# Kernel optimization log

Measured on AMD Instinct MI355X. Metric: run time of the kernel, lower is better.

The kernel has to match this reference:

```python
import jax, jax.numpy as jnp
import numpy as np

N, E, D, ED, H = 4096, 262144, 256, 64, 8
HD = D // H


def _ln(x, g, b, eps=1e-5):
    mu = jnp.mean(x, axis=-1, keepdims=True)
    var = jnp.mean((x - mu) ** 2, axis=-1, keepdims=True)
    return (x - mu) * jax.lax.rsqrt(var + eps) * g + b


def setup_inputs() -> dict:
    key = jax.random.key(0)
    ks = jax.random.split(key, 16)
    p = lambda k, s: (0.02 * jax.random.normal(k, s, dtype=jnp.float32))
    return {
        'x': jax.random.normal(ks[0], (N, D), dtype=jnp.float32),
        'edge_index': jax.random.randint(ks[1], (2, E), 0, N, dtype=jnp.int64),
        'edge_attr': jax.random.normal(ks[2], (E, ED), dtype=jnp.float32),
        'eps': jnp.zeros((), dtype=jnp.float32),  # GINEConv train_eps initial value 0
        'Wl': p(ks[3], (ED, D)), 'bl': jnp.zeros((D,), jnp.float32),
        'W1': p(ks[4], (D, D)), 'b1': jnp.zeros((D,), jnp.float32),
        'W2': p(ks[5], (D, D)), 'b2': jnp.zeros((D,), jnp.float32),
        'ln_l_g': jnp.ones((D,), jnp.float32), 'ln_l_b': jnp.zeros((D,), jnp.float32),
        'in_w': p(ks[6], (3 * D, D)), 'in_b': jnp.zeros((3 * D,), jnp.float32),
        'out_w': p(ks[7], (D, D)), 'out_b': jnp.zeros((D,), jnp.float32),
        'ln_a_g': jnp.ones((D,), jnp.float32), 'ln_a_b': jnp.zeros((D,), jnp.float32),
        'Wf1': p(ks[8], (D, 2 * D)), 'bf1': jnp.zeros((2 * D,), jnp.float32),
        'Wf2': p(ks[9], (2 * D, D)), 'bf2': jnp.zeros((D,), jnp.float32),
        'ln_f_g': jnp.ones((D,), jnp.float32), 'ln_f_b': jnp.zeros((D,), jnp.float32),
    }


def reference(x, edge_index, edge_attr, eps, Wl, bl, W1, b1, W2, b2,
              ln_l_g, ln_l_b, in_w, in_b, out_w, out_b, ln_a_g, ln_a_b,
              Wf1, bf1, Wf2, bf2, ln_f_g, ln_f_b):
    n = x.shape[0]
    src, dst = edge_index[0], edge_index[1]
    # --- GINEConv: msg = relu(x_j + lin(edge_attr)), sum-aggregate, MLP((1+eps)x + agg)
    msg = jax.nn.relu(x[src] + edge_attr @ Wl + bl)            # [E, D]
    agg = jax.ops.segment_sum(msg, dst, num_segments=n)        # [N, D]
    h = (1.0 + eps) * x + agg
    h = jax.nn.elu(h @ W1 + b1) @ W2 + b2                      # local_mlp
    x = x + jax.nn.elu(_ln(h, ln_l_g, ln_l_b))                 # local residual (dropout=eval)
    # --- MultiheadAttention (single batch of all nodes)
    qkv = x @ in_w.T + in_b                                    # [N, 3D]
    q, k, v = jnp.split(qkv, 3, axis=-1)
    q = q.reshape(n, H, HD)
    k = k.reshape(n, H, HD)
    v = v.reshape(n, H, HD)
    scores = jnp.einsum('qhd,khd->hqk', q, k) / jnp.sqrt(jnp.float32(HD))
    attn = jax.nn.softmax(scores, axis=-1)
    o = jnp.einsum('hqk,khd->qhd', attn, v).reshape(n, D)
    o = o @ out_w.T + out_b
    x = x + _ln(o, ln_a_g, ln_a_b)
    # --- FFN (exact GELU as in torch nn.GELU default)
    f = jax.nn.gelu(x @ Wf1 + bf1, approximate=False) @ Wf2 + bf2
    x = x + _ln(f, ln_f_g, ln_f_b)
    return x
```

## Files before the change

kernel.cpp:

```cpp
#include <hip/hip_runtime.h>
#include <cstddef>

#define D 256
#define H 8
#define HD 32
#define ED 64
#define TPB 4

typedef __attribute__((ext_vector_type(8))) short short8;
typedef __attribute__((ext_vector_type(4))) short short4v;
typedef __attribute__((ext_vector_type(4))) float floatx4;

__device__ inline short f2bf(float f) {
    unsigned u = __float_as_uint(f);
    unsigned r = (u + 0x7fffu + ((u >> 16) & 1u)) >> 16;
    return (short)r;
}

template<int ACT> __device__ inline float act_f(float v) {
    if (ACT == 1) return fmaxf(v, 0.f);
    if (ACT == 2) return v > 0.f ? v : expm1f(v);
    if (ACT == 3) return 0.5f * v * (1.f + erff(v * 0.70710678118654752f));
    return v;
}

__device__ inline float wave_sum(float v) {
#pragma unroll
    for (int off = 32; off > 0; off >>= 1) v += __shfl_xor(v, off, 64);
    return v;
}

__global__ void prep_kernel(
        const float* __restrict__ Wl, const float* __restrict__ W1,
        const float* __restrict__ W2, const float* __restrict__ in_w,
        const float* __restrict__ outw, const float* __restrict__ Wf1,
        const float* __restrict__ Wf2, const float* __restrict__ x,
        const float* __restrict__ eps,
        short* __restrict__ WlT, short* __restrict__ W1bt, short* __restrict__ W2bt,
        short* __restrict__ inwbt, short* __restrict__ outwbt,
        short* __restrict__ Wf1bt, short* __restrict__ Wf2bt,
        int* __restrict__ cnt, float* __restrict__ h, int N, int NF) {
    int idx = blockIdx.x * 256 + threadIdx.x;
    if (idx < 16384) { int n = idx >> 6, k = idx & 63; WlT[idx] = f2bf(Wl[k * 256 + n]); return; }
    idx -= 16384;
    if (idx < 65536) { int n = idx >> 8, k = idx & 255; W1bt[idx] = f2bf(W1[k * 256 + n]); return; }
    idx -= 65536;
    if (idx < 65536) { int n = idx >> 8, k = idx & 255; W2bt[idx] = f2bf(W2[k * 256 + n]); return; }
    idx -= 65536;
    if (idx < 196608) { inwbt[idx] = f2bf(in_w[idx]); return; }
    idx -= 196608;
    if (idx < 65536) { outwbt[idx] = f2bf(outw[idx]); return; }
    idx -= 65536;
    if (idx < 131072) { int n = idx >> 8, k = idx & 255; Wf1bt[idx] = f2bf(Wf1[k * 512 + n]); return; }
    idx -= 131072;
    if (idx < 131072) { int n = idx >> 9, k = idx & 511; Wf2bt[idx] = f2bf(Wf2[k * 256 + n]); return; }
    idx -= 131072;
    if (idx < N) { cnt[idx] = 0; return; }
    idx -= N;
    if (idx < NF) { h[idx] = (1.f + eps[0]) * x[idx]; }
}

__global__ void hist_kernel(const int* __restrict__ ei, int* __restrict__ cnt, int E) {
    int e = blockIdx.x * 256 + threadIdx.x;
    if (e < E) atomicAdd(&cnt[ei[E + e]], 1);
}

__global__ __launch_bounds__(1024) void scan_kernel(int* __restrict__ cnt,
                                                    int* __restrict__ offs) {
    __shared__ int s[1024];
    int tid = threadIdx.x;
    int4 c = *(int4*)&cnt[tid * 4];
    int sum = c.x + c.y + c.z + c.w;
    s[tid] = sum;
    __syncthreads();
    for (int off = 1; off < 1024; off <<= 1) {
        int v = (tid >= off) ? s[tid - off] : 0;
        __syncthreads();
        s[tid] += v;
        __syncthreads();
    }
    int ex = s[tid] - sum;
    int o1 = ex + c.x, o2 = o1 + c.y, o3 = o2 + c.z;
    offs[tid * 4] = ex; offs[tid * 4 + 1] = o1;
    offs[tid * 4 + 2] = o2; offs[tid * 4 + 3] = o3;
    cnt[tid * 4] = ex; cnt[tid * 4 + 1] = o1;
    cnt[tid * 4 + 2] = o2; cnt[tid * 4 + 3] = o3;
    if (tid == 1023) offs[4096] = s[1023];
}

__global__ void scatter_kernel(const int* __restrict__ ei, int* __restrict__ cursor,
                               int* __restrict__ perm, int* __restrict__ srcp,
                               int* __restrict__ dstp, int E) {
    int e = blockIdx.x * 256 + threadIdx.x;
    if (e < E) {
        int d = ei[E + e];
        int pos = atomicAdd(&cursor[d], 1);
        perm[pos] = e;
        srcp[pos] = ei[e];
        dstp[pos] = d;
    }
}

__global__ __launch_bounds__(256) void edge_fused_kernel(
        const float* __restrict__ ea, const short* __restrict__ WlT,
        const float* __restrict__ bl, const float* __restrict__ x,
        const int* __restrict__ perm, const int* __restrict__ srcp,
        const int* __restrict__ dstp, float* __restrict__ h) {
    __shared__ __align__(16) short ea_s[2][64 * 72];
    int tid = threadIdx.x;
    int wave = tid >> 6, lane = tid & 63;
    int mm = lane & 15, quad = lane >> 4;
    int base_e = blockIdx.x * (64 * TPB);

    int myperm[TPB], mysrc[TPB], mydst[TPB];
#pragma unroll
    for (int t = 0; t < TPB; t++) {
        myperm[t] = perm[base_e + t * 64 + lane];
        mysrc[t]  = srcp[base_e + t * 64 + lane];
        mydst[t]  = dstp[base_e + t * 64 + lane];
    }
    short8 af[4][2];
#pragma unroll
    for (int t = 0; t < 4; t++)
#pragma unroll
        for (int q2 = 0; q2 < 2; q2++)
            af[t][q2] = *(const short8*)&WlT[(wave * 64 + t * 16 + mm) * 64 + q2 * 32 + quad * 8];
    float4 blv[4];
#pragma unroll
    for (int t = 0; t < 4; t++)
        blv[t] = *(const float4*)&bl[wave * 64 + t * 16 + quad * 4];

    {
        float4 r[4];
#pragma unroll
        for (int p = 0; p < 4; p++) {
            int slot = tid + p * 256;
            int row = slot >> 4, c4 = slot & 15;
            int prow = __shfl(myperm[0], row);
            r[p] = *(const float4*)&ea[(size_t)prow * ED + c4 * 4];
        }
#pragma unroll
        for (int p = 0; p < 4; p++) {
            int slot = tid + p * 256;
            int row = slot >> 4, c4 = slot & 15;
            short4v s; s[0] = f2bf(r[p].x); s[1] = f2bf(r[p].y); s[2] = f2bf(r[p].z); s[3] = f2bf(r[p].w);
            *(short4v*)&ea_s[0][row * 72 + c4 * 4] = s;
        }
    }
    __syncthreads();

#pragma unroll
    for (int t = 0; t < TPB; t++) {
        const int buf = t & 1;
        float4 pre[4];
        if (t + 1 < TPB) {
#pragma unroll
            for (int p = 0; p < 4; p++) {
                int slot = tid + p * 256;
                int row = slot >> 4, c4 = slot & 15;
                int prow = __shfl(myperm[t + 1], row);
                pre[p] = *(const float4*)&ea[(size_t)prow * ED + c4 * 4];
            }
        }
        floatx4 acc[4][4];
#pragma unroll
        for (int et = 0; et < 4; et++)
#pragma unroll
            for (int tt = 0; tt < 4; tt++) acc[et][tt] = (floatx4){0.f, 0.f, 0.f, 0.f};
#pragma unroll
        for (int et = 0; et < 4; et++) {
            short8 bf0 = *(const short8*)&ea_s[buf][(et * 16 + mm) * 72 + quad * 8];
            short8 bf1 = *(const short8*)&ea_s[buf][(et * 16 + mm) * 72 + 32 + quad * 8];
#pragma unroll
            for (int tt = 0; tt < 4; tt++) {
                acc[et][tt] = __builtin_amdgcn_mfma_f32_16x16x32_bf16(af[tt][0], bf0, acc[et][tt], 0, 0, 0);
                acc[et][tt] = __builtin_amdgcn_mfma_f32_16x16x32_bf16(af[tt][1], bf1, acc[et][tt], 0, 0, 0);
            }
        }
#pragma unroll
        for (int et = 0; et < 4; et++) {
            int srci = __shfl(mysrc[t], et * 16 + mm);
            const float* xrow = x + (size_t)srci * D + wave * 64 + quad * 4;
#pragma unroll
            for (int tt = 0; tt < 4; tt++) {
                float4 xv = *(const float4*)(xrow + tt * 16);
                acc[et][tt][0] = fmaxf(acc[et][tt][0] + blv[tt].x + xv.x, 0.f);
                acc[et][tt][1] = fmaxf(acc[et][tt][1] + blv[tt].y + xv.y, 0.f);
                acc[et][tt][2] = fmaxf(acc[et][tt][2] + blv[tt].z + xv.z, 0.f);
                acc[et][tt][3] = fmaxf(acc[et][tt][3] + blv[tt].w + xv.w, 0.f);
            }
        }
        int prevd = __shfl_up(mydst[t], 1);
        bool bnd = (lane == 0) || (mydst[t] != prevd);
        unsigned long long m = __ballot(bnd);
        while (m) {
            int segstart = (int)__builtin_ctzll(m);
            m &= m - 1;
            int segend = m ? (int)__builtin_ctzll(m) : 64;
            int segdst = __shfl(mydst[t], segstart);
            bool in0 = (0 * 16 + mm >= segstart) & (0 * 16 + mm < segend);
            bool in1 = (1 * 16 + mm >= segstart) & (1 * 16 + mm < segend);
            bool in2 = (2 * 16 + mm >= segstart) & (2 * 16 + mm < segend);
            bool in3 = (3 * 16 + mm >= segstart) & (3 * 16 + mm < segend);
            float* hrow = h + (size_t)segdst * D + wave * 64;
#pragma unroll
            for (int tt = 0; tt < 4; tt++) {
#pragma unroll
                for (int j = 0; j < 4; j++) {
                    float v = (in0 ? acc[0][tt][j] : 0.f) + (in1 ? acc[1][tt][j] : 0.f)
                            + (in2 ? acc[2][tt][j] : 0.f) + (in3 ? acc[3][tt][j] : 0.f);
                    v += __shfl_xor(v, 1);
                    v += __shfl_xor(v, 2);
                    v += __shfl_xor(v, 4);
                    v += __shfl_xor(v, 8);
                    if (mm == 0) atomicAdd(&hrow[tt * 16 + quad * 4 + j], v);
                }
            }
        }
        if (t + 1 < TPB) {
#pragma unroll
            for (int p = 0; p < 4; p++) {
                int slot = tid + p * 256;
                int row = slot >> 4, c4 = slot & 15;
                short4v s; s[0] = f2bf(pre[p].x); s[1] = f2bf(pre[p].y);
                s[2] = f2bf(pre[p].z); s[3] = f2bf(pre[p].w);
                *(short4v*)&ea_s[1 - buf][row * 72 + c4 * 4] = s;
            }
            __syncthreads();
        }
    }
}

#define GSTR 40
template<int ACT>
__global__ __launch_bounds__(256) void gemm_bf16_kernel(
        const float* __restrict__ A, const short* __restrict__ Bt,
        const float* __restrict__ bias, float* __restrict__ C,
        int M, int K, int Nc) {
    __shared__ __align__(16) short As[64 * GSTR];
    __shared__ __align__(16) short Bs[64 * GSTR];
    int tid = threadIdx.x;
    int wave = tid >> 6, lane = tid & 63;
    int mm = lane & 15, quad = lane >> 4;
    int wm = wave >> 1, wn = wave & 1;
    int m0 = blockIdx.y * 64, n0 = blockIdx.x * 64;
    floatx4 acc[2][2];
#pragma unroll
    for (int i = 0; i < 2; i++)
#pragma unroll
        for (int j = 0; j < 2; j++) acc[i][j] = (floatx4){0.f, 0.f, 0.f, 0.f};
    for (int k0 = 0; k0 < K; k0 += 32) {
#pragma unroll
        for (int p = 0; p < 2; p++) {
            int slot = tid + p * 256;
            int row = slot >> 3, c4 = slot & 7;
            float4 v = *(const float4*)&A[(size_t)(m0 + row) * K + k0 + c4 * 4];
            short4v s; s[0] = f2bf(v.x); s[1] = f2bf(v.y); s[2] = f2bf(v.z); s[3] = f2bf(v.w);
            *(short4v*)&As[row * GSTR + c4 * 4] = s;
        }
        {
            int row = tid >> 2, seg = tid & 3;
            short8 v = *(const short8*)&Bt[(size_t)(n0 + row) * K + k0 + seg * 8];
            *(short8*)&Bs[row * GSTR + seg * 8] = v;
        }
        __syncthreads();
        short8 af[2], bf[2];
#pragma unroll
        for (int t = 0; t < 2; t++) {
            af[t] = *(const short8*)&As[(wm * 32 + t * 16 + mm) * GSTR + quad * 8];
            bf[t] = *(const short8*)&Bs[(wn * 32 + t * 16 + mm) * GSTR + quad * 8];
        }
#pragma unroll
        for (int i = 0; i < 2; i++)
#pragma unroll
            for (int j = 0; j < 2; j++)
                acc[i][j] = __builtin_amdgcn_mfma_f32_16x16x32_bf16(af[i], bf[j], acc[i][j], 0, 0, 0);
        __syncthreads();
    }
#pragma unroll
    for (int i = 0; i < 2; i++) {
#pragma unroll
        for (int j = 0; j < 2; j++) {
            int ncol = n0 + wn * 32 + j * 16 + mm;
            float bv = bias[ncol];
#pragma unroll
            for (int r = 0; r < 4; r++) {
                int mrow = m0 + wm * 32 + i * 16 + quad * 4 + r;
                C[(size_t)mrow * Nc + ncol] = act_f<ACT>(acc[i][j][r] + bv);
            }
        }
    }
}

template<int ACT>
__global__ __launch_bounds__(256) void ln_res_kernel(
        const float* __restrict__ t, const float* __restrict__ res,
        const float* __restrict__ g, const float* __restrict__ b,
        float* __restrict__ out) {
    __shared__ float red[8];
    int row = blockIdx.x, tid = threadIdx.x;
    float v = t[(size_t)row * D + tid];
    int wid = tid >> 6, lane = tid & 63;
    float s = wave_sum(v);
    if (lane == 0) red[wid] = s;
    __syncthreads();
    float mu = (red[0] + red[1] + red[2] + red[3]) * (1.f / D);
    float dv = v - mu;
    float s2 = wave_sum(dv * dv);
    if (lane == 0) red[4 + wid] = s2;
    __syncthreads();
    float var = (red[4] + red[5] + red[6] + red[7]) * (1.f / D);
    float y = dv * rsqrtf(var + 1e-5f) * g[tid] + b[tid];
    y = act_f<ACT>(y);
    out[(size_t)row * D + tid] = res[(size_t)row * D + tid] + y;
}

#define KSTR 40
#define VSTR 136
#define ATILE 128
__global__ __launch_bounds__(256) void attn_mfma_kernel(
        const float* __restrict__ qkv, float* __restrict__ po,
        float* __restrict__ pm, float* __restrict__ pl, int N, int KC_) {
    __shared__ __align__(16) short Ks[ATILE * KSTR];
    __shared__ __align__(16) short VTs[HD * VSTR];
    const int tid = threadIdx.x;
    const int wave = tid >> 6, lane = tid & 63;
    const int mm = lane & 15, quad = lane >> 4;
    const int h = blockIdx.y, c = blockIdx.z;
    const int qbase = blockIdx.x * 64 + wave * 16;
    const float scale = 0.17677669529663687f;

    short8 qf;
    {
        const float* qrow = qkv + (size_t)(qbase + mm) * (3 * D) + h * HD + quad * 8;
        float4 a = *(const float4*)qrow;
        float4 b = *(const float4*)(qrow + 4);
        qf[0] = f2bf(a.x * scale); qf[1] = f2bf(a.y * scale);
        qf[2] = f2bf(a.z * scale); qf[3] = f2bf(a.w * scale);
        qf[4] = f2bf(b.x * scale); qf[5] = f2bf(b.y * scale);
        qf[6] = f2bf(b.z * scale); qf[7] = f2bf(b.w * scale);
    }
    floatx4 accA = {0.f, 0.f, 0.f, 0.f};
    floatx4 accB = {0.f, 0.f, 0.f, 0.f};
    float m_r = -1e30f, l_r = 0.f;

    const int kchunk = N / KC_;
    const int kstart = c * kchunk;
    const int krow0 = ((mm >> 2) << 3) | (mm & 3);

    for (int t0 = 0; t0 < kchunk; t0 += ATILE) {
#pragma unroll
        for (int p = 0; p < 4; p++) {
            int slot = tid + p * 256;
            int kr = slot >> 3, e4 = slot & 7;
            const float* krow = qkv + (size_t)(kstart + t0 + kr) * (3 * D) + D + h * HD + e4 * 4;
            float4 kv = *(const float4*)krow;
            short4v ks;
            ks[0] = f2bf(kv.x); ks[1] = f2bf(kv.y); ks[2] = f2bf(kv.z); ks[3] = f2bf(kv.w);
            *(short4v*)&Ks[kr * KSTR + e4 * 4] = ks;
            const float* vrow = qkv + (size_t)(kstart + t0 + kr) * (3 * D) + 2 * D + h * HD + e4 * 4;
            float4 vv = *(const float4*)vrow;
            VTs[(e4 * 4 + 0) * VSTR + kr] = f2bf(vv.x);
            VTs[(e4 * 4 + 1) * VSTR + kr] = f2bf(vv.y);
            VTs[(e4 * 4 + 2) * VSTR + kr] = f2bf(vv.z);
            VTs[(e4 * 4 + 3) * VSTR + kr] = f2bf(vv.w);
        }
        __syncthreads();
#pragma unroll
        for (int s = 0; s < ATILE / 32; s++) {
            int sb = s * 32;
            short8 kf0 = *(const short8*)&Ks[(sb + krow0) * KSTR + quad * 8];
            short8 kf1 = *(const short8*)&Ks[(sb + krow0 + 4) * KSTR + quad * 8];
            floatx4 zero = {0.f, 0.f, 0.f, 0.f};
            floatx4 s0 = __builtin_amdgcn_mfma_f32_16x16x32_bf16(kf0, qf, zero, 0, 0, 0);
            floatx4 s1 = __builtin_amdgcn_mfma_f32_16x16x32_bf16(kf1, qf, zero, 0, 0, 0);
            float mx = fmaxf(fmaxf(fmaxf(s0[0], s0[1]), fmaxf(s0[2], s0[3])),
                             fmaxf(fmaxf(s1[0], s1[1]), fmaxf(s1[2], s1[3])));
            mx = fmaxf(mx, __shfl_xor(mx, 16));
            mx = fmaxf(mx, __shfl_xor(mx, 32));
            float nm = fmaxf(m_r, mx);
            float alpha = __expf(m_r - nm);
            float p0[4], p1[4], ls = 0.f;
#pragma unroll
            for (int j = 0; j < 4; j++) {
                p0[j] = __expf(s0[j] - nm);
                p1[j] = __expf(s1[j] - nm);
                ls += p0[j] + p1[j];
            }
            ls += __shfl_xor(ls, 16);
            ls += __shfl_xor(ls, 32);
            l_r = l_r * alpha + ls;
            m_r = nm;
            short8 pf;
#pragma unroll
            for (int j = 0; j < 4; j++) { pf[j] = f2bf(p0[j]); pf[4 + j] = f2bf(p1[j]); }
#pragma unroll
            for (int j = 0; j < 4; j++) { accA[j] *= alpha; accB[j] *= alpha; }
            short8 vf0 = *(const short8*)&VTs[mm * VSTR + sb + quad * 8];
            short8 vf1 = *(const short8*)&VTs[(mm + 16) * VSTR + sb + quad * 8];
            accA = __builtin_amdgcn_mfma_f32_16x16x32_bf16(vf0, pf, accA, 0, 0, 0);
            accB = __builtin_amdgcn_mfma_f32_16x16x32_bf16(vf1, pf, accB, 0, 0, 0);
        }
        __syncthreads();
    }
    size_t NH = (size_t)N * H;
    int qi = qbase + mm;
    size_t nh = (size_t)qi * H + h;
    if (lane < 16) {
        pm[(size_t)c * NH + nh] = m_r;
        pl[(size_t)c * NH + nh] = l_r;
    }
    float* op = po + ((size_t)c * NH + nh) * HD;
#pragma unroll
    for (int j = 0; j < 4; j++) {
        op[quad * 4 + j] = accA[j];
        op[16 + quad * 4 + j] = accB[j];
    }
}

__global__ __launch_bounds__(256) void attn_combine_kernel(
        const float* __restrict__ po, const float* __restrict__ pm,
        const float* __restrict__ pl, float* __restrict__ obuf, int N, int KC_) {
    int idx = blockIdx.x * 256 + threadIdx.x;
    int d = idx & (HD - 1);
    int nh = idx >> 5;
    size_t NH = (size_t)N * H;
    float M = -1e30f;
    for (int cc = 0; cc < KC_; cc++) M = fmaxf(M, pm[(size_t)cc * NH + nh]);
    float l = 0.f, o = 0.f;
    for (int cc = 0; cc < KC_; cc++) {
        float a = __expf(pm[(size_t)cc * NH + nh] - M);
        l += a * pl[(size_t)cc * NH + nh];
        o += a * po[((size_t)cc * NH + nh) * HD + d];
    }
    int n = nh >> 3, h = nh & (H - 1);
    obuf[(size_t)n * D + h * HD + d] = o / l;
}

extern "C" void kernel_launch(void* const* d_in, const int* in_sizes, int n_in,
                              void* d_out, int out_size, void* d_ws, size_t ws_size,
                              hipStream_t stream) {
    const float* x    = (const float*)d_in[0];
    const int*   ei   = (const int*)d_in[1];
    const float* ea   = (const float*)d_in[2];
    const float* eps  = (const float*)d_in[3];
    const float* Wl   = (const float*)d_in[4];
    const float* bl   = (const float*)d_in[5];
    const float* W1   = (const float*)d_in[6];
    const float* b1   = (const float*)d_in[7];
    const float* W2   = (const float*)d_in[8];
    const float* b2   = (const float*)d_in[9];
    const float* lnlg = (const float*)d_in[10];
    const float* lnlb = (const float*)d_in[11];
    const float* in_w = (const float*)d_in[12];
    const float* in_b = (const float*)d_in[13];
    const float* outw = (const float*)d_in[14];
    const float* outb = (const float*)d_in[15];
    const float* lnag = (const float*)d_in[16];
    const float* lnab = (const float*)d_in[17];
    const float* Wf1  = (const float*)d_in[18];
    const float* bf1  = (const float*)d_in[19];
    const float* Wf2  = (const float*)d_in[20];
    const float* bf2  = (const float*)d_in[21];
    const float* lnfg = (const float*)d_in[22];
    const float* lnfb = (const float*)d_in[23];
    float* out = (float*)d_out;

    const int N = in_sizes[0] / D;
    const int E = in_sizes[1] / 2;
    const size_t NF = (size_t)N * D;
    const size_t NH = (size_t)N * H;

    const int KCsel = 4;
    size_t floatEnd = (4 + (size_t)KCsel) * NF + 2 * (size_t)KCsel * NH;
    size_t offB = (floatEnd * 4 + 15) & ~(size_t)15;
    size_t intCount = (size_t)N + 3 * (size_t)E + (size_t)(N + 1);
    size_t wltOff = (offB + intCount * 4 + 15) & ~(size_t)15;

    float* w = (float*)d_ws;
    float* x1   = w;
    float* qkv  = w + NF;
    float* h    = w + 4 * NF;
    float* t1   = w + 5 * NF;
    float* t2   = w + 6 * NF;
    float* po   = w + 4 * NF;
    float* pm   = w + (4 + (size_t)KCsel) * NF;
    float* pl   = pm + (size_t)KCsel * NH;
    float* obuf = w + NF;
    float* t3   = w + 2 * NF;
    float* x2   = w + 3 * NF;
    float* f1   = w + 4 * NF;
    float* f2   = w + 6 * NF;

    char* base = (char*)d_ws;
    int* ibase  = (int*)(base + offB);
    int* cnt    = ibase;
    int* perm   = ibase + N;
    int* srcp   = perm + E;
    int* dstp   = srcp + E;
    int* offs   = dstp + E;
    short* WlT    = (short*)(base + wltOff);
    short* W1bt   = WlT + 16384;
    short* W2bt   = W1bt + 65536;
    short* inwbt  = W2bt + 65536;
    short* outwbt = inwbt + 196608;
    short* Wf1bt  = outwbt + 65536;
    short* Wf2bt  = Wf1bt + 131072;

    {
        int total = 671744 + N + (int)NF;
        prep_kernel<<<(total + 255) / 256, 256, 0, stream>>>(
            Wl, W1, W2, in_w, outw, Wf1, Wf2, x, eps,
            WlT, W1bt, W2bt, inwbt, outwbt, Wf1bt, Wf2bt, cnt, h, N, (int)NF);
    }
    hist_kernel<<<(E + 255) / 256, 256, 0, stream>>>(ei, cnt, E);
    scan_kernel<<<1, 1024, 0, stream>>>(cnt, offs);
    scatter_kernel<<<(E + 255) / 256, 256, 0, stream>>>(ei, cnt, perm, srcp, dstp, E);
    edge_fused_kernel<<<E / (64 * TPB), 256, 0, stream>>>(ea, WlT, bl, x, perm, srcp, dstp, h);
    gemm_bf16_kernel<2><<<dim3(D / 64, N / 64), 256, 0, stream>>>(h, W1bt, b1, t1, N, D, D);
    gemm_bf16_kernel<0><<<dim3(D / 64, N / 64), 256, 0, stream>>>(t1, W2bt, b2, t2, N, D, D);
    ln_res_kernel<2><<<N, 256, 0, stream>>>(t2, x, lnlg, lnlb, x1);
    gemm_bf16_kernel<0><<<dim3(3 * D / 64, N / 64), 256, 0, stream>>>(x1, inwbt, in_b, qkv, N, D, 3 * D);
    attn_mfma_kernel<<<dim3(N / 64, H, KCsel), 256, 0, stream>>>(qkv, po, pm, pl, N, KCsel);
    attn_combine_kernel<<<(int)(NF / 256), 256, 0, stream>>>(po, pm, pl, obuf, N, KCsel);
    gemm_bf16_kernel<0><<<dim3(D / 64, N / 64), 256, 0, stream>>>(obuf, outwbt, outb, t3, N, D, D);
    ln_res_kernel<0><<<N, 256, 0, stream>>>(t3, x1, lnag, lnab, x2);
    gemm_bf16_kernel<3><<<dim3(2 * D / 64, N / 64), 256, 0, stream>>>(x2, Wf1bt, bf1, f1, N, D, 2 * D);
    gemm_bf16_kernel<0><<<dim3(D / 64, N / 64), 256, 0, stream>>>(f1, Wf2bt, bf2, f2, N, 2 * D, D);
    ln_res_kernel<0><<<N, 256, 0, stream>>>(f2, x2, lnfg, lnfb, out);

    (void)n_in; (void)out_size; (void)ws_size;
}
```

Before: 426.5 us.

## Process four query fragments per attention wave and widen GEMM K-tile

Each attention wave now handles 64 queries (four 16-row fragments) instead of 16. Every K/V tile staged in shared memory is therefore reused four times, which cuts the global fp32-to-bf16 staging work per query. The key split is raised from 4 to 8 chunks to keep enough blocks in flight, at the cost of larger partial buffers and more work in the combine step. Separately, the bf16 GEMM now steps through K in tiles of 64 rather than 32, halving the number of barriers and loop iterations, with a larger LDS row stride.

```diff
diff --git a/kernel.cpp b/kernel.cpp
--- a/kernel.cpp
+++ b/kernel.cpp
@@ -231,7 +231,7 @@
     }
 }
 
-#define GSTR 40
+#define GSTR 72
 template<int ACT>
 __global__ __launch_bounds__(256) void gemm_bf16_kernel(
         const float* __restrict__ A, const short* __restrict__ Bt,
@@ -249,32 +249,38 @@
     for (int i = 0; i < 2; i++)
 #pragma unroll
         for (int j = 0; j < 2; j++) acc[i][j] = (floatx4){0.f, 0.f, 0.f, 0.f};
-    for (int k0 = 0; k0 < K; k0 += 32) {
-#pragma unroll
-        for (int p = 0; p < 2; p++) {
+    for (int k0 = 0; k0 < K; k0 += 64) {
+#pragma unroll
+        for (int p = 0; p < 4; p++) {
             int slot = tid + p * 256;
-            int row = slot >> 3, c4 = slot & 7;
+            int row = slot >> 4, c4 = slot & 15;
             float4 v = *(const float4*)&A[(size_t)(m0 + row) * K + k0 + c4 * 4];
             short4v s; s[0] = f2bf(v.x); s[1] = f2bf(v.y); s[2] = f2bf(v.z); s[3] = f2bf(v.w);
             *(short4v*)&As[row * GSTR + c4 * 4] = s;
         }
-        {
-            int row = tid >> 2, seg = tid & 3;
+#pragma unroll
+        for (int p = 0; p < 2; p++) {
+            int slot = tid + p * 256;
+            int row = slot >> 3, seg = slot & 7;
             short8 v = *(const short8*)&Bt[(size_t)(n0 + row) * K + k0 + seg * 8];
             *(short8*)&Bs[row * GSTR + seg * 8] = v;
         }
         __syncthreads();
-        short8 af[2], bf[2];
-#pragma unroll
-        for (int t = 0; t < 2; t++) {
-            af[t] = *(const short8*)&As[(wm * 32 + t * 16 + mm) * GSTR + quad * 8];
-            bf[t] = *(const short8*)&Bs[(wn * 32 + t * 16 + mm) * GSTR + quad * 8];
-        }
+        short8 af[2][2], bf[2][2];
+#pragma unroll
+        for (int t = 0; t < 2; t++)
+#pragma unroll
+            for (int q2 = 0; q2 < 2; q2++) {
+                af[t][q2] = *(const short8*)&As[(wm * 32 + t * 16 + mm) * GSTR + q2 * 32 + quad * 8];
+                bf[t][q2] = *(const short8*)&Bs[(wn * 32 + t * 16 + mm) * GSTR + q2 * 32 + quad * 8];
+            }
 #pragma unroll
         for (int i = 0; i < 2; i++)
 #pragma unroll
-            for (int j = 0; j < 2; j++)
-                acc[i][j] = __builtin_amdgcn_mfma_f32_16x16x32_bf16(af[i], bf[j], acc[i][j], 0, 0, 0);
+            for (int j = 0; j < 2; j++) {
+                acc[i][j] = __builtin_amdgcn_mfma_f32_16x16x32_bf16(af[i][0], bf[j][0], acc[i][j], 0, 0, 0);
+                acc[i][j] = __builtin_amdgcn_mfma_f32_16x16x32_bf16(af[i][1], bf[j][1], acc[i][j], 0, 0, 0);
+            }
         __syncthreads();
     }
 #pragma unroll
@@ -318,6 +324,7 @@
 #define KSTR 40
 #define VSTR 136
 #define ATILE 128
+#define AQF 4
 __global__ __launch_bounds__(256) void attn_mfma_kernel(
         const float* __restrict__ qkv, float* __restrict__ po,
         float* __restrict__ pm, float* __restrict__ pl, int N, int KC_) {
@@ -327,22 +334,28 @@
     const int wave = tid >> 6, lane = tid & 63;
     const int mm = lane & 15, quad = lane >> 4;
     const int h = blockIdx.y, c = blockIdx.z;
-    const int qbase = blockIdx.x * 64 + wave * 16;
+    const int qbase = blockIdx.x * 256 + wave * 64;
     const float scale = 0.17677669529663687f;
 
-    short8 qf;
-    {
-        const float* qrow = qkv + (size_t)(qbase + mm) * (3 * D) + h * HD + quad * 8;
+    short8 qf[AQF];
+#pragma unroll
+    for (int f = 0; f < AQF; f++) {
+        const float* qrow = qkv + (size_t)(qbase + f * 16 + mm) * (3 * D) + h * HD + quad * 8;
         float4 a = *(const float4*)qrow;
         float4 b = *(const float4*)(qrow + 4);
-        qf[0] = f2bf(a.x * scale); qf[1] = f2bf(a.y * scale);
-        qf[2] = f2bf(a.z * scale); qf[3] = f2bf(a.w * scale);
-        qf[4] = f2bf(b.x * scale); qf[5] = f2bf(b.y * scale);
-        qf[6] = f2bf(b.z * scale); qf[7] = f2bf(b.w * scale);
-    }
-    floatx4 accA = {0.f, 0.f, 0.f, 0.f};
-    floatx4 accB = {0.f, 0.f, 0.f, 0.f};
-    float m_r = -1e30f, l_r = 0.f;
+        qf[f][0] = f2bf(a.x * scale); qf[f][1] = f2bf(a.y * scale);
+        qf[f][2] = f2bf(a.z * scale); qf[f][3] = f2bf(a.w * scale);
+        qf[f][4] = f2bf(b.x * scale); qf[f][5] = f2bf(b.y * scale);
+        qf[f][6] = f2bf(b.z * scale); qf[f][7] = f2bf(b.w * scale);
+    }
+    floatx4 accA[AQF], accB[AQF];
+    float m_r[AQF], l_r[AQF];
+#pragma unroll
+    for (int f = 0; f < AQF; f++) {
+        accA[f] = (floatx4){0.f, 0.f, 0.f, 0.f};
+        accB[f] = (floatx4){0.f, 0.f, 0.f, 0.f};
+        m_r[f] = -1e30f; l_r[f] = 0.f;
+    }
 
     const int kchunk = N / KC_;
     const int kstart = c * kchunk;
@@ -371,50 +384,56 @@
             int sb = s * 32;
             short8 kf0 = *(const short8*)&Ks[(sb + krow0) * KSTR + quad * 8];
             short8 kf1 = *(const short8*)&Ks[(sb + krow0 + 4) * KSTR + quad * 8];
-            floatx4 zero = {0.f, 0.f, 0.f, 0.f};
-            floatx4 s0 = __builtin_amdgcn_mfma_f32_16x16x32_bf16(kf0, qf, zero, 0, 0, 0);
-            floatx4 s1 = __builtin_amdgcn_mfma_f32_16x16x32_bf16(kf1, qf, zero, 0, 0, 0);
-            float mx = fmaxf(fmaxf(fmaxf(s0[0], s0[1]), fmaxf(s0[2], s0[3])),
-                             fmaxf(fmaxf(s1[0], s1[1]), fmaxf(s1[2], s1[3])));
-            mx = fmaxf(mx, __shfl_xor(mx, 16));
-            mx = fmaxf(mx, __shfl_xor(mx, 32));
-            float nm = fmaxf(m_r, mx);
-            float alpha = __expf(m_r - nm);
-            float p0[4], p1[4], ls = 0.f;
-#pragma unroll
-            for (int j = 0; j < 4; j++) {
-                p0[j] = __expf(s0[j] - nm);
-                p1[j] = __expf(s1[j] - nm);
-                ls += p0[j] + p1[j];
-            }
-            ls += __shfl_xor(ls, 16);
-            ls += __shfl_xor(ls, 32);
-            l_r = l_r * alpha + ls;
-            m_r = nm;
-            short8 pf;
-#pragma unroll
-            for (int j = 0; j < 4; j++) { pf[j] = f2bf(p0[j]); pf[4 + j] = f2bf(p1[j]); }
-#pragma unroll
-            for (int j = 0; j < 4; j++) { accA[j] *= alpha; accB[j] *= alpha; }
             short8 vf0 = *(const short8*)&VTs[mm * VSTR + sb + quad * 8];
             short8 vf1 = *(const short8*)&VTs[(mm + 16) * VSTR + sb + quad * 8];
-            accA = __builtin_amdgcn_mfma_f32_16x16x32_bf16(vf0, pf, accA, 0, 0, 0);
-            accB = __builtin_amdgcn_mfma_f32_16x16x32_bf16(vf1, pf, accB, 0, 0, 0);
+            floatx4 zero = {0.f, 0.f, 0.f, 0.f};
+#pragma unroll
+            for (int f = 0; f < AQF; f++) {
+                floatx4 s0 = __builtin_amdgcn_mfma_f32_16x16x32_bf16(kf0, qf[f], zero, 0, 0, 0);
+                floatx4 s1 = __builtin_amdgcn_mfma_f32_16x16x32_bf16(kf1, qf[f], zero, 0, 0, 0);
+                float mx = fmaxf(fmaxf(fmaxf(s0[0], s0[1]), fmaxf(s0[2], s0[3])),
+                                 fmaxf(fmaxf(s1[0], s1[1]), fmaxf(s1[2], s1[3])));
+                mx = fmaxf(mx, __shfl_xor(mx, 16));
+                mx = fmaxf(mx, __shfl_xor(mx, 32));
+                float nm = fmaxf(m_r[f], mx);
+                float alpha = __expf(m_r[f] - nm);
+                float p0[4], p1[4], ls = 0.f;
+#pragma unroll
+                for (int j = 0; j < 4; j++) {
+                    p0[j] = __expf(s0[j] - nm);
+                    p1[j] = __expf(s1[j] - nm);
+                    ls += p0[j] + p1[j];
+                }
+                ls += __shfl_xor(ls, 16);
+                ls += __shfl_xor(ls, 32);
+                l_r[f] = l_r[f] * alpha + ls;
+                m_r[f] = nm;
+                short8 pf;
+#pragma unroll
+                for (int j = 0; j < 4; j++) { pf[j] = f2bf(p0[j]); pf[4 + j] = f2bf(p1[j]); }
+#pragma unroll
+                for (int j = 0; j < 4; j++) { accA[f][j] *= alpha; accB[f][j] *= alpha; }
+                accA[f] = __builtin_amdgcn_mfma_f32_16x16x32_bf16(vf0, pf, accA[f], 0, 0, 0);
+                accB[f] = __builtin_amdgcn_mfma_f32_16x16x32_bf16(vf1, pf, accB[f], 0, 0, 0);
+            }
         }
         __syncthreads();
     }
     size_t NH = (size_t)N * H;
-    int qi = qbase + mm;
-    size_t nh = (size_t)qi * H + h;
-    if (lane < 16) {
-        pm[(size_t)c * NH + nh] = m_r;
-        pl[(size_t)c * NH + nh] = l_r;
-    }
-    float* op = po + ((size_t)c * NH + nh) * HD;
-#pragma unroll
-    for (int j = 0; j < 4; j++) {
-        op[quad * 4 + j] = accA[j];
-        op[16 + quad * 4 + j] = accB[j];
+#pragma unroll
+    for (int f = 0; f < AQF; f++) {
+        int qi = qbase + f * 16 + mm;
+        size_t nh = (size_t)qi * H + h;
+        if (lane < 16) {
+            pm[(size_t)c * NH + nh] = m_r[f];
+            pl[(size_t)c * NH + nh] = l_r[f];
+        }
+        float* op = po + ((size_t)c * NH + nh) * HD;
+#pragma unroll
+        for (int j = 0; j < 4; j++) {
+            op[quad * 4 + j] = accA[f][j];
+            op[16 + quad * 4 + j] = accB[f][j];
+        }
     }
 }
 
@@ -471,7 +490,7 @@
     const size_t NF = (size_t)N * D;
     const size_t NH = (size_t)N * H;
 
-    const int KCsel = 4;
+    const int KCsel = 8;
     size_t floatEnd = (4 + (size_t)KCsel) * NF + 2 * (size_t)KCsel * NH;
     size_t offB = (floatEnd * 4 + 15) & ~(size_t)15;
     size_t intCount = (size_t)N + 3 * (size_t)E + (size_t)(N + 1);
@@ -521,7 +540,7 @@
     gemm_bf16_kernel<0><<<dim3(D / 64, N / 64), 256, 0, stream>>>(t1, W2bt, b2, t2, N, D, D);
     ln_res_kernel<2><<<N, 256, 0, stream>>>(t2, x, lnlg, lnlb, x1);
     gemm_bf16_kernel<0><<<dim3(3 * D / 64, N / 64), 256, 0, stream>>>(x1, inwbt, in_b, qkv, N, D, 3 * D);
-    attn_mfma_kernel<<<dim3(N / 64, H, KCsel), 256, 0, stream>>>(qkv, po, pm, pl, N, KCsel);
+    attn_mfma_kernel<<<dim3(N / 256, H, KCsel), 256, 0, stream>>>(qkv, po, pm, pl, N, KCsel);
     attn_combine_kernel<<<(int)(NF / 256), 256, 0, stream>>>(po, pm, pl, obuf, N, KCsel);
     gemm_bf16_kernel<0><<<dim3(D / 64, N / 64), 256, 0, stream>>>(obuf, outwbt, outb, t3, N, D, D);
     ln_res_kernel<0><<<N, 256, 0, stream>>>(t3, x1, lnag, lnab, x2);
```

After: 454.4 us. 6.6% more time.
